# Optimization experiments

Hardware: AMD Instinct MI355X
Metric: run time of the kernel (lower is better)

The kernel has to match this reference:

```python
import jax, jax.numpy as jnp
import numpy as np

HEADS = 8
DIM_HEAD = 64
EPS = 1e-5


def setup_inputs() -> dict:
    key = jax.random.key(0)
    k1, k2, k3, k4 = jax.random.split(key, 4)
    dim, hidden = 256, HEADS * DIM_HEAD
    x = jax.random.normal(k1, (16, dim, 64, 64), dtype=jnp.float32)
    w_qkv = jax.random.normal(k2, (hidden * 3, dim), dtype=jnp.float32) * (dim ** -0.5)
    w_out = jax.random.normal(k3, (dim, hidden), dtype=jnp.float32) * (hidden ** -0.5)
    b_out = jax.random.normal(k4, (dim,), dtype=jnp.float32) * 0.01
    g = jnp.ones((dim,), dtype=jnp.float32)
    return {"x": x, "w_qkv": w_qkv, "w_out": w_out, "b_out": b_out, "g": g}


def reference(x, w_qkv, w_out, b_out, g):
    b, c, H, W = x.shape
    n = H * W
    scale = DIM_HEAD ** -0.5
    xf = x.reshape(b, c, n)
    # 1x1 conv == channel GEMM
    qkv = jnp.einsum('oc,bcn->bon', w_qkv, xf)          # [b, 3*hidden, n]
    q, k, v = jnp.split(qkv, 3, axis=1)
    hd = (b, HEADS, DIM_HEAD, n)
    q = q.reshape(hd)
    k = k.reshape(hd)
    v = v.reshape(hd)
    q = jax.nn.softmax(q, axis=2) * scale               # softmax over head-channel d
    k = jax.nn.softmax(k, axis=3)                       # softmax over tokens n
    v = v / n
    context = jnp.einsum('bhdn,bhen->bhde', k, v)       # [b,h,d,e], d=e=DIM_HEAD
    out = jnp.einsum('bhde,bhdn->bhen', context, q)     # [b,h,e,n]
    out = out.reshape(b, HEADS * DIM_HEAD, n)
    y = jnp.einsum('oc,bcn->bon', w_out, out) + b_out[None, :, None]
    # LayerNorm over channel dim (biased var, eps for fp32)
    mean = jnp.mean(y, axis=1, keepdims=True)
    var = jnp.mean((y - mean) ** 2, axis=1, keepdims=True)
    y = (y - mean) * jax.lax.rsqrt(var + EPS) * g[None, :, None]
    return y.reshape(b, c, H, W)
```

## Files before the change

kernel.cpp:

```cpp
#include <hip/hip_runtime.h>
#include <hip/hip_bf16.h>
#include <cstddef>
#include <cstdint>


typedef __attribute__((ext_vector_type(8))) short s16x8;
typedef __attribute__((ext_vector_type(4))) float f32x4;

#define MFMA(a,b,c) __builtin_amdgcn_mfma_f32_16x16x32_bf16(a,b,c,0,0,0)

#define XT_BSTRIDE 1048576

__device__ __forceinline__ unsigned short f2bf(float f){
    union { float f; unsigned int u; } v; v.f = f;
    unsigned int u = v.u;
    unsigned int r = (u + 0x7FFFu + ((u >> 16) & 1u)) >> 16;
    return (unsigned short)r;
}
__device__ __forceinline__ float bf2f(unsigned short b){
    union { unsigned int u; float f; } v; v.u = ((unsigned int)b) << 16;
    return v.f;
}
__device__ __forceinline__ unsigned int pack2bf(float a, float b){
    __hip_bfloat162 h = __float22bfloat162_rn(make_float2(a, b));
    union { __hip_bfloat162 h; unsigned int u; } v; v.h = h;
    return v.u;
}
__device__ __forceinline__ void gload_lds16(const void* g, void* l){
    __builtin_amdgcn_global_load_lds(
        (const __attribute__((address_space(1))) unsigned int*)g,
        (__attribute__((address_space(3))) unsigned int*)l, 16, 0, 0);
}

__global__ __launch_bounds__(256)
void xprep_kernel(const float* __restrict__ x, unsigned short* __restrict__ XT)
{
    __shared__ float xt[64*68];
    const int tid = threadIdx.x;
    const int n0 = blockIdx.x * 64;
    const int c0 = blockIdx.y * 64;
    const int b  = blockIdx.z;
    {
        const int ci = tid >> 2, ng = tid & 3;
        const float* xs = x + (size_t)b*1048576 + (size_t)(c0+ci)*4096 + n0 + ng*16;
        #pragma unroll
        for (int k=0;k<4;++k){
            float4 v = *(const float4*)(xs + k*4);
            *(float4*)&xt[ci*68 + ng*16 + k*4] = v;
        }
    }
    __syncthreads();
    const int nr = tid >> 2, cg = tid & 3;
    const int n = n0 + nr;
    unsigned short* dstrow = XT + (size_t)b*XT_BSTRIDE + (size_t)n*256;
    #pragma unroll
    for (int t2=0;t2<2;++t2){
        s16x8 pk;
        #pragma unroll
        for (int j=0;j<8;++j){
            int c = cg*16 + t2*8 + j;
            pk[j] = (short)f2bf(xt[c*68 + nr]);
        }
        int blk = (((c0>>3) + cg*2 + t2) ^ (n & 7));
        *(s16x8*)(dstrow + blk*8) = pk;
    }
}

__global__ __launch_bounds__(256)
void wprep_kernel(const float* __restrict__ w, unsigned short* __restrict__ wb)
{
    int i = (blockIdx.x*256 + threadIdx.x) * 8;
    float4 a = *(const float4*)(w + i);
    float4 b = *(const float4*)(w + i + 4);
    s16x8 pk;
    pk[0]=(short)f2bf(a.x); pk[1]=(short)f2bf(a.y); pk[2]=(short)f2bf(a.z); pk[3]=(short)f2bf(a.w);
    pk[4]=(short)f2bf(b.x); pk[5]=(short)f2bf(b.y); pk[6]=(short)f2bf(b.z); pk[7]=(short)f2bf(b.w);
    *(s16x8*)(wb + i) = pk;
}

__global__ __launch_bounds__(256)
void wqprep_kernel(const float* __restrict__ w, unsigned short* __restrict__ wqp)
{
    int t = blockIdx.x*256 + threadIdx.x;
    int row = t >> 5, c8 = t & 31;
    int kc = c8 >> 2, q = c8 & 3;
    const float* src = w + (size_t)row*256 + c8*8;
    float4 a = *(const float4*)(src);
    float4 b = *(const float4*)(src + 4);
    s16x8 pk;
    pk[0]=(short)f2bf(a.x); pk[1]=(short)f2bf(a.y); pk[2]=(short)f2bf(a.z); pk[3]=(short)f2bf(a.w);
    pk[4]=(short)f2bf(b.x); pk[5]=(short)f2bf(b.y); pk[6]=(short)f2bf(b.z); pk[7]=(short)f2bf(b.w);
    *(s16x8*)(wqp + ((size_t)(kc*512 + row)*4 + q)*8) = pk;
}

__global__ __launch_bounds__(256,2)
void kvctx_kernel(const unsigned short* __restrict__ XT, const unsigned short* __restrict__ wb,
                  float* __restrict__ Cp, float* __restrict__ Zp)
{
    extern __shared__ char smraw[];
    unsigned short* xtile = (unsigned short*)smraw;
    unsigned short* kv    = (unsigned short*)(smraw + 32768);

    const int tid = threadIdx.x;
    const int w = tid >> 6, lane = tid & 63;
    const int l15 = lane & 15, q = lane >> 4;
    const int flat = blockIdx.x;
    const int qb  = flat & 63;
    const int h   = flat >> 6;
    const int b   = qb >> 2;
    const int seg = qb & 3;
    const int bh  = b*8 + h;

    s16x8 aW[2][8];
    #pragma unroll
    for (int mf=0;mf<2;++mf){
        int rl = w*16 + l15;
        int grow = (mf==0) ? (512 + h*64 + rl) : (1024 + h*64 + rl);
        const unsigned short* wr = wb + (size_t)grow*256 + q*8;
        #pragma unroll
        for (int kc=0;kc<8;++kc)
            aW[mf][kc] = *(const s16x8*)(wr + kc*32);
    }

    f32x4 ctxacc[4];
    #pragma unroll
    for (int ef=0;ef<4;++ef) ctxacc[ef] = (f32x4){0.f,0.f,0.f,0.f};
    float zacc[4];
    #pragma unroll
    for (int i=0;i<4;++i) zacc[i]=0.f;

    const unsigned short* gsrc0 = XT + (size_t)b*XT_BSTRIDE + (size_t)(seg*1024)*256;

    {
        const unsigned short* gs = gsrc0 + w*4096 + lane*8;
        #pragma unroll
        for (int j=0;j<8;++j)
            gload_lds16(gs + j*512, &xtile[w*4096 + j*512]);
    }
    __syncthreads();

    #pragma unroll 1
    for (int t=0;t<16;++t){
        f32x4 acc[2][4];
        #pragma unroll
        for (int mf=0;mf<2;++mf)
            #pragma unroll
            for (int nf=0;nf<4;++nf) acc[mf][nf]=(f32x4){0.f,0.f,0.f,0.f};
        #pragma unroll
        for (int kc=0;kc<8;++kc){
            s16x8 bf[4];
            #pragma unroll
            for (int nf=0;nf<4;++nf){
                int nl = nf*16 + l15;
                int blk = (kc*4 + q) ^ (nl & 7);
                bf[nf] = *(const s16x8*)&xtile[nl*256 + blk*8];
            }
            #pragma unroll
            for (int mf=0;mf<2;++mf)
                #pragma unroll
                for (int nf=0;nf<4;++nf)
                    acc[mf][nf] = MFMA(aW[mf][kc], bf[nf], acc[mf][nf]);
        }
        #pragma unroll
        for (int mf=0;mf<2;++mf){
            int row = ((mf==0) ? (w*16) : (64 + w*16)) + q*4;
            #pragma unroll
            for (int nf=0;nf<4;++nf){
                int col = nf*16 + l15;
                #pragma unroll
                for (int r=0;r<4;++r){
                    float v = acc[mf][nf][r];
                    unsigned short bv;
                    if (mf == 0){
                        v = __expf(v);
                        bv = f2bf(v);
                        zacc[r] += bf2f(bv);
                    } else {
                        bv = f2bf(v);
                    }
                    kv[(row+r)*72 + col] = bv;
                }
            }
        }
        __syncthreads();
        if (t < 15){
            const unsigned short* gs = gsrc0 + (t+1)*16384 + w*4096 + lane*8;
            #pragma unroll
            for (int j=0;j<8;++j)
                gload_lds16(gs + j*512, &xtile[w*4096 + j*512]);
        }
        #pragma unroll
        for (int kf=0;kf<2;++kf){
            s16x8 aC = *(const s16x8*)&kv[(w*16 + l15)*72 + kf*32 + q*8];
            #pragma unroll
            for (int ef=0;ef<4;++ef){
                s16x8 bC = *(const s16x8*)&kv[(64 + ef*16 + l15)*72 + kf*32 + q*8];
                ctxacc[ef] = MFMA(aC, bC, ctxacc[ef]);
            }
        }
        __syncthreads();
    }

    float* cpb = Cp + (size_t)(bh*4 + seg)*4096;
    #pragma unroll
    for (int ef=0;ef<4;++ef)
        #pragma unroll
        for (int r=0;r<4;++r){
            int d = w*16 + q*4 + r;
            cpb[d*64 + ef*16 + l15] = ctxacc[ef][r];
        }
    #pragma unroll
    for (int i=0;i<4;++i){
        #pragma unroll
        for (int off=1; off<16; off<<=1)
            zacc[i] += __shfl_xor(zacc[i], off, 64);
    }
    if (l15 == 0){
        float* zpb = Zp + (size_t)(bh*4 + seg)*64;
        #pragma unroll
        for (int r=0;r<4;++r)
            zpb[w*16 + q*4 + r] = zacc[r];
    }
}

__global__ __launch_bounds__(512)
void ctxu_kernel(const float* __restrict__ Cp, const float* __restrict__ Zp,
                 const float* __restrict__ wout, unsigned short* __restrict__ U)
{
    extern __shared__ char smraw[];
    float* wl = (float*)smraw;
    float* cl = (float*)(smraw + 69632);
    const int h = blockIdx.x, b = blockIdx.y, tid = threadIdx.x;
    const int bh = b*8 + h;
    {
        const int r = tid >> 1, half = tid & 1;
        const float* wsrc = wout + (size_t)r*512 + h*64 + half*32;
        #pragma unroll
        for (int j=0;j<8;++j){
            float4 v = *(const float4*)(wsrc + j*4);
            *(float4*)&wl[r*68 + half*32 + j*4] = v;
        }
    }
    {
        const int d = tid >> 3, e0 = (tid & 7) * 8;
        float zs = 0.f;
        #pragma unroll
        for (int s=0;s<4;++s) zs += Zp[(bh*4+s)*64 + d];
        float zv = 1.f / (zs * 4096.f);
        const float* cb = Cp + (size_t)(bh*4)*4096 + d*64 + e0;
        float v[8];
        #pragma unroll
        for (int j=0;j<8;++j) v[j]=0.f;
        #pragma unroll
        for (int s=0;s<4;++s){
            float4 t0 = *(const float4*)(cb + (size_t)s*4096);
            float4 t1 = *(const float4*)(cb + (size_t)s*4096 + 4);
            v[0]+=t0.x; v[1]+=t0.y; v[2]+=t0.z; v[3]+=t0.w;
            v[4]+=t1.x; v[5]+=t1.y; v[6]+=t1.z; v[7]+=t1.w;
        }
        #pragma unroll
        for (int j=0;j<8;++j) cl[d*68 + e0 + j] = v[j] * zv;
    }
    __syncthreads();
    const int o = tid & 255, dg = tid >> 8;
    float wlr[64];
    #pragma unroll
    for (int j=0;j<16;++j){
        float4 v = *(const float4*)&wl[o*68 + j*4];
        wlr[j*4+0]=v.x; wlr[j*4+1]=v.y; wlr[j*4+2]=v.z; wlr[j*4+3]=v.w;
    }
    float outv[32];
    #pragma unroll 1
    for (int dd=0;dd<32;++dd){
        const int d = dg*32 + dd;
        float s = 0.f;
        #pragma unroll
        for (int j=0;j<16;++j){
            float4 c4 = *(const float4*)&cl[d*68 + j*4];
            s += wlr[j*4+0]*c4.x + wlr[j*4+1]*c4.y + wlr[j*4+2]*c4.z + wlr[j*4+3]*c4.w;
        }
        outv[dd] = s * 0.125f;
    }
    const int kc = h*2 + dg;
    unsigned short* ub = U + (size_t)b*131072 + (size_t)(kc*256 + o)*32;
    #pragma unroll
    for (int g4=0; g4<4; ++g4){
        uint4 pk;
        pk.x = pack2bf(outv[g4*8+0], outv[g4*8+1]);
        pk.y = pack2bf(outv[g4*8+2], outv[g4*8+3]);
        pk.z = pack2bf(outv[g4*8+4], outv[g4*8+5]);
        pk.w = pack2bf(outv[g4*8+6], outv[g4*8+7]);
        *(uint4*)(ub + g4*8) = pk;
    }
}

__global__ __launch_bounds__(512,4)
void qout_kernel(const unsigned short* __restrict__ XT, const unsigned short* __restrict__ wqp,
                 const unsigned short* __restrict__ U, const float* __restrict__ bout,
                 const float* __restrict__ gg, float* __restrict__ out)
{
    extern __shared__ char smraw[];
    unsigned short* xtile = (unsigned short*)smraw;
    unsigned short* qsm   = (unsigned short*)smraw;
    float* red = (float*)(smraw + 66560);
    float* bl  = (float*)(smraw + 70656);
    float* gl  = (float*)(smraw + 71680);

    const int tid = threadIdx.x;
    const int w = tid >> 6, lane = tid & 63, l15 = lane & 15, q = lane >> 4;
    const int b = blockIdx.y;
    const int n0 = blockIdx.x * 64;

    if (tid < 256){
        bl[tid] = bout[tid];
        gl[tid] = gg[tid];
    }
    {
        const unsigned short* gs = XT + (size_t)b*XT_BSTRIDE + (size_t)n0*256 + w*2048 + lane*8;
        #pragma unroll
        for (int j=0;j<4;++j)
            gload_lds16(gs + j*512, &xtile[w*2048 + j*512]);
    }
    const unsigned short* wqb = wqp + (size_t)q*8 + (size_t)(w*64 + l15)*32;
    s16x8 av0[4];
    #pragma unroll
    for (int mf=0;mf<4;++mf)
        av0[mf] = *(const s16x8*)(wqb + (size_t)mf*16*32);
    __syncthreads();

    f32x4 acc[4][4];
    #pragma unroll
    for (int mf=0;mf<4;++mf)
        #pragma unroll
        for (int nf=0;nf<4;++nf) acc[mf][nf]=(f32x4){0.f,0.f,0.f,0.f};

    #pragma unroll
    for (int kc=0; kc<8; ++kc){
        s16x8 av[4];
        #pragma unroll
        for (int mf=0;mf<4;++mf)
            av[mf] = (kc == 0) ? av0[mf]
                               : *(const s16x8*)(wqb + (size_t)kc*512*32 + (size_t)mf*16*32);
        s16x8 bf[4];
        #pragma unroll
        for (int nf=0;nf<4;++nf){
            int nl = nf*16 + l15;
            int blk = (kc*4 + q) ^ (nl & 7);
            bf[nf] = *(const s16x8*)&xtile[nl*256 + blk*8];
        }
        __builtin_amdgcn_s_setprio(1);
        #pragma unroll
        for (int mf=0;mf<4;++mf)
            #pragma unroll
            for (int nf=0;nf<4;++nf)
                acc[mf][nf] = MFMA(av[mf], bf[nf], acc[mf][nf]);
        __builtin_amdgcn_s_setprio(0);
    }

    #pragma unroll
    for (int nf=0;nf<4;++nf){
        float m = -1e30f;
        #pragma unroll
        for (int mf=0;mf<4;++mf)
            #pragma unroll
            for (int r=0;r<4;++r)
                m = fmaxf(m, acc[mf][nf][r]);
        m = fmaxf(m, __shfl_xor(m, 16, 64));
        m = fmaxf(m, __shfl_xor(m, 32, 64));
        float s = 0.f;
        #pragma unroll
        for (int mf=0;mf<4;++mf)
            #pragma unroll
            for (int r=0;r<4;++r){
                float e = __expf(acc[mf][nf][r] - m);
                acc[mf][nf][r] = e;
                s += e;
            }
        s += __shfl_xor(s, 16, 64);
        s += __shfl_xor(s, 32, 64);
        float rs = 1.f / s;
        #pragma unroll
        for (int mf=0;mf<4;++mf)
            #pragma unroll
            for (int r=0;r<4;++r)
                acc[mf][nf][r] *= rs;
    }
    __syncthreads();

    #pragma unroll
    for (int mf=0;mf<4;++mf){
        int dbase = w*64 + mf*16 + q*4;
        #pragma unroll
        for (int nf=0;nf<4;++nf){
            int n = nf*16 + l15;
            unsigned int lo = pack2bf(acc[mf][nf][0], acc[mf][nf][1]);
            unsigned int hi = pack2bf(acc[mf][nf][2], acc[mf][nf][3]);
            *(uint2*)&qsm[n*520 + dbase] = make_uint2(lo, hi);
        }
    }
    const unsigned short* Ub = U + (size_t)b*131072 + (size_t)q*8 + (size_t)(w*32 + l15)*32;
    s16x8 uvP[4];
    #pragma unroll
    for (int i=0;i<4;++i)
        uvP[i] = *(const s16x8*)(Ub + (size_t)(i>>1)*256*32 + (size_t)(i&1)*16*32);
    __syncthreads();

    f32x4 yacc[2][4];
    #pragma unroll
    for (int mf=0;mf<2;++mf)
        #pragma unroll
        for (int nf=0;nf<4;++nf) yacc[mf][nf]=(f32x4){0.f,0.f,0.f,0.f};

    #pragma unroll
    for (int kc=0; kc<16; ++kc){
        s16x8 uv[2];
        #pragma unroll
        for (int mf=0;mf<2;++mf)
            uv[mf] = (kc < 2) ? uvP[(kc<<1)|mf]
                              : *(const s16x8*)(Ub + (size_t)kc*256*32 + (size_t)mf*16*32);
        s16x8 bf[4];
        #pragma unroll
        for (int nf=0;nf<4;++nf){
            int n = nf*16 + l15;
            bf[nf] = *(const s16x8*)&qsm[n*520 + kc*32 + q*8];
        }
        __builtin_amdgcn_s_setprio(1);
        #pragma unroll
        for (int mf=0;mf<2;++mf)
            #pragma unroll
            for (int nf=0;nf<4;++nf)
                yacc[mf][nf] = MFMA(uv[mf], bf[nf], yacc[mf][nf]);
        __builtin_amdgcn_s_setprio(0);
    }

    #pragma unroll
    for (int mf=0;mf<2;++mf){
        int ob = w*32 + mf*16 + q*4;
        #pragma unroll
        for (int r=0;r<4;++r){
            float bo = bl[ob + r];
            #pragma unroll
            for (int nf=0;nf<4;++nf) yacc[mf][nf][r] += bo;
        }
    }
    float s1[4], s2[4];
    #pragma unroll
    for (int nf=0;nf<4;++nf){ s1[nf]=0.f; s2[nf]=0.f; }
    #pragma unroll
    for (int mf=0;mf<2;++mf)
        #pragma unroll
        for (int nf=0;nf<4;++nf)
            #pragma unroll
            for (int r=0;r<4;++r){
                float v = yacc[mf][nf][r];
                s1[nf] += v; s2[nf] += v*v;
            }
    #pragma unroll
    for (int nf=0;nf<4;++nf){
        s1[nf] += __shfl_xor(s1[nf], 16, 64);
        s1[nf] += __shfl_xor(s1[nf], 32, 64);
        s2[nf] += __shfl_xor(s2[nf], 16, 64);
        s2[nf] += __shfl_xor(s2[nf], 32, 64);
    }
    if (q == 0){
        #pragma unroll
        for (int nf=0;nf<4;++nf){
            int col = nf*16 + l15;
            red[(w*64 + col)*2 + 0] = s1[nf];
            red[(w*64 + col)*2 + 1] = s2[nf];
        }
    }
    __syncthreads();
    float mean_[4], inv_[4];
    #pragma unroll
    for (int nf=0;nf<4;++nf){
        int col = nf*16 + l15;
        float S1 = 0.f, S2 = 0.f;
        #pragma unroll
        for (int w2=0; w2<8; ++w2){
            S1 += red[(w2*64 + col)*2 + 0];
            S2 += red[(w2*64 + col)*2 + 1];
        }
        float mn = S1 * (1.f/256.f);
        float vr = S2 * (1.f/256.f) - mn*mn;
        mean_[nf] = mn;
        inv_[nf] = rsqrtf(vr + 1e-5f);
    }
    float* ob = out + (size_t)b*1048576 + n0;
    #pragma unroll
    for (int mf=0;mf<2;++mf){
        #pragma unroll
        for (int r=0;r<4;++r){
            int o = w*32 + mf*16 + q*4 + r;
            float gv = gl[o];
            #pragma unroll
            for (int nf=0;nf<4;++nf){
                float val = (yacc[mf][nf][r] - mean_[nf]) * inv_[nf] * gv;
                ob[(size_t)o*4096 + nf*16 + l15] = val;
            }
        }
    }
}

extern "C" void kernel_launch(void* const* d_in, const int* in_sizes, int n_in,
                              void* d_out, int out_size, void* d_ws, size_t ws_size,
                              hipStream_t stream)
{
    const float* x    = (const float*)d_in[0];
    const float* wqkv = (const float*)d_in[1];
    const float* wout = (const float*)d_in[2];
    const float* bout = (const float*)d_in[3];
    const float* g    = (const float*)d_in[4];
    float* out = (float*)d_out;

    char* wsb = (char*)d_ws;
    unsigned short* XTs = (unsigned short*)wsb;
    unsigned short* wbf = (unsigned short*)(wsb + 33554432);
    unsigned short* Upk = (unsigned short*)(wsb + 34340864);
    float* Cp  = (float*)(wsb + 38535168);
    float* Zp  = (float*)(wsb + 46923776);
    unsigned short* wqp = (unsigned short*)(wsb + 47054848);

    hipLaunchKernelGGL(xprep_kernel,  dim3(64, 4, 16), dim3(256), 0,     stream, x, XTs);
    hipLaunchKernelGGL(wprep_kernel,  dim3(192),       dim3(256), 0,     stream, wqkv, wbf);
    hipLaunchKernelGGL(wqprep_kernel, dim3(64),        dim3(256), 0,     stream, wqkv, wqp);
    hipLaunchKernelGGL(kvctx_kernel,  dim3(512),       dim3(256), 51200, stream, XTs, wbf, Cp, Zp);
    hipLaunchKernelGGL(ctxu_kernel,   dim3(8, 16),     dim3(512), 87040, stream, Cp, Zp, wout, Upk);
    hipLaunchKernelGGL(qout_kernel,   dim3(64, 16),    dim3(512), 72704, stream, XTs, wqp, Upk, bout, g, out);
}
```

Measured before the change: 138.0 us.

## Split kvctx work across 8 waves: separate K and V projection waves

The kvctx kernel moves from 256 to 512 threads per block. Waves 0-3 compute the K projection (exp and row-sum) and waves 4-7 compute the V projection, where before each wave did both. The context MFMA is split by output column halves across the two wave groups. This halves per-wave register use and MFMA work, adding latency hiding and parallelism within each block, at the cost of more waves contending for LDS and the same barrier count.

After: 146.4 us. 1.06x slower.

```diff
diff --git a/kernel.cpp b/kernel.cpp
--- a/kernel.cpp
+++ b/kernel.cpp
@@ -93,7 +93,7 @@
     *(s16x8*)(wqp + ((size_t)(kc*512 + row)*4 + q)*8) = pk;
 }
 
-__global__ __launch_bounds__(256,2)
+__global__ __launch_bounds__(512,4)
 void kvctx_kernel(const unsigned short* __restrict__ XT, const unsigned short* __restrict__ wb,
                   float* __restrict__ Cp, float* __restrict__ Zp)
 {
@@ -104,6 +104,8 @@
     const int tid = threadIdx.x;
     const int w = tid >> 6, lane = tid & 63;
     const int l15 = lane & 15, q = lane >> 4;
+    const int isK = (w < 4);
+    const int wf  = w & 3;
     const int flat = blockIdx.x;
     const int qb  = flat & 63;
     const int h   = flat >> 6;
@@ -111,20 +113,19 @@
     const int seg = qb & 3;
     const int bh  = b*8 + h;
 
-    s16x8 aW[2][8];
-    #pragma unroll
-    for (int mf=0;mf<2;++mf){
-        int rl = w*16 + l15;
-        int grow = (mf==0) ? (512 + h*64 + rl) : (1024 + h*64 + rl);
+    s16x8 aW[8];
+    {
+        int rl = wf*16 + l15;
+        int grow = isK ? (512 + h*64 + rl) : (1024 + h*64 + rl);
         const unsigned short* wr = wb + (size_t)grow*256 + q*8;
         #pragma unroll
         for (int kc=0;kc<8;++kc)
-            aW[mf][kc] = *(const s16x8*)(wr + kc*32);
-    }
-
-    f32x4 ctxacc[4];
-    #pragma unroll
-    for (int ef=0;ef<4;++ef) ctxacc[ef] = (f32x4){0.f,0.f,0.f,0.f};
+            aW[kc] = *(const s16x8*)(wr + kc*32);
+    }
+
+    f32x4 ctxacc[2];
+    ctxacc[0]=(f32x4){0.f,0.f,0.f,0.f};
+    ctxacc[1]=(f32x4){0.f,0.f,0.f,0.f};
     float zacc[4];
     #pragma unroll
     for (int i=0;i<4;++i) zacc[i]=0.f;
@@ -132,20 +133,18 @@
     const unsigned short* gsrc0 = XT + (size_t)b*XT_BSTRIDE + (size_t)(seg*1024)*256;
 
     {
-        const unsigned short* gs = gsrc0 + w*4096 + lane*8;
-        #pragma unroll
-        for (int j=0;j<8;++j)
-            gload_lds16(gs + j*512, &xtile[w*4096 + j*512]);
+        const unsigned short* gs = gsrc0 + w*2048 + lane*8;
+        #pragma unroll
+        for (int j=0;j<4;++j)
+            gload_lds16(gs + j*512, &xtile[w*2048 + j*512]);
     }
     __syncthreads();
 
     #pragma unroll 1
     for (int t=0;t<16;++t){
-        f32x4 acc[2][4];
-        #pragma unroll
-        for (int mf=0;mf<2;++mf)
-            #pragma unroll
-            for (int nf=0;nf<4;++nf) acc[mf][nf]=(f32x4){0.f,0.f,0.f,0.f};
+        f32x4 acc[4];
+        #pragma unroll
+        for (int nf=0;nf<4;++nf) acc[nf]=(f32x4){0.f,0.f,0.f,0.f};
         #pragma unroll
         for (int kc=0;kc<8;++kc){
             s16x8 bf[4];
@@ -156,22 +155,19 @@
                 bf[nf] = *(const s16x8*)&xtile[nl*256 + blk*8];
             }
             #pragma unroll
-            for (int mf=0;mf<2;++mf)
-                #pragma unroll
-                for (int nf=0;nf<4;++nf)
-                    acc[mf][nf] = MFMA(aW[mf][kc], bf[nf], acc[mf][nf]);
-        }
-        #pragma unroll
-        for (int mf=0;mf<2;++mf){
-            int row = ((mf==0) ? (w*16) : (64 + w*16)) + q*4;
+            for (int nf=0;nf<4;++nf)
+                acc[nf] = MFMA(aW[kc], bf[nf], acc[nf]);
+        }
+        {
+            int row = (isK ? (wf*16) : (64 + wf*16)) + q*4;
             #pragma unroll
             for (int nf=0;nf<4;++nf){
                 int col = nf*16 + l15;
                 #pragma unroll
                 for (int r=0;r<4;++r){
-                    float v = acc[mf][nf][r];
+                    float v = acc[nf][r];
                     unsigned short bv;
-                    if (mf == 0){
+                    if (isK){
                         v = __expf(v);
                         bv = f2bf(v);
                         zacc[r] += bf2f(bv);
@@ -184,17 +180,18 @@
         }
         __syncthreads();
         if (t < 15){
-            const unsigned short* gs = gsrc0 + (t+1)*16384 + w*4096 + lane*8;
-            #pragma unroll
-            for (int j=0;j<8;++j)
-                gload_lds16(gs + j*512, &xtile[w*4096 + j*512]);
+            const unsigned short* gs = gsrc0 + (t+1)*16384 + w*2048 + lane*8;
+            #pragma unroll
+            for (int j=0;j<4;++j)
+                gload_lds16(gs + j*512, &xtile[w*2048 + j*512]);
         }
         #pragma unroll
         for (int kf=0;kf<2;++kf){
-            s16x8 aC = *(const s16x8*)&kv[(w*16 + l15)*72 + kf*32 + q*8];
-            #pragma unroll
-            for (int ef=0;ef<4;++ef){
-                s16x8 bC = *(const s16x8*)&kv[(64 + ef*16 + l15)*72 + kf*32 + q*8];
+            s16x8 aC = *(const s16x8*)&kv[(wf*16 + l15)*72 + kf*32 + q*8];
+            #pragma unroll
+            for (int ef=0;ef<2;++ef){
+                int e = (w>>2)*32 + ef*16 + l15;
+                s16x8 bC = *(const s16x8*)&kv[(64 + e)*72 + kf*32 + q*8];
                 ctxacc[ef] = MFMA(aC, bC, ctxacc[ef]);
             }
         }
@@ -203,23 +200,26 @@
 
     float* cpb = Cp + (size_t)(bh*4 + seg)*4096;
     #pragma unroll
-    for (int ef=0;ef<4;++ef)
+    for (int ef=0;ef<2;++ef)
         #pragma unroll
         for (int r=0;r<4;++r){
-            int d = w*16 + q*4 + r;
-            cpb[d*64 + ef*16 + l15] = ctxacc[ef][r];
-        }
-    #pragma unroll
-    for (int i=0;i<4;++i){
-        #pragma unroll
-        for (int off=1; off<16; off<<=1)
-            zacc[i] += __shfl_xor(zacc[i], off, 64);
-    }
-    if (l15 == 0){
-        float* zpb = Zp + (size_t)(bh*4 + seg)*64;
-        #pragma unroll
-        for (int r=0;r<4;++r)
-            zpb[w*16 + q*4 + r] = zacc[r];
+            int d = wf*16 + q*4 + r;
+            int e = (w>>2)*32 + ef*16 + l15;
+            cpb[d*64 + e] = ctxacc[ef][r];
+        }
+    if (isK){
+        #pragma unroll
+        for (int i=0;i<4;++i){
+            #pragma unroll
+            for (int off=1; off<16; off<<=1)
+                zacc[i] += __shfl_xor(zacc[i], off, 64);
+        }
+        if (l15 == 0){
+            float* zpb = Zp + (size_t)(bh*4 + seg)*64;
+            #pragma unroll
+            for (int r=0;r<4;++r)
+                zpb[wf*16 + q*4 + r] = zacc[r];
+        }
     }
 }
 
@@ -524,7 +524,7 @@
     hipLaunchKernelGGL(xprep_kernel,  dim3(64, 4, 16), dim3(256), 0,     stream, x, XTs);
     hipLaunchKernelGGL(wprep_kernel,  dim3(192),       dim3(256), 0,     stream, wqkv, wbf);
     hipLaunchKernelGGL(wqprep_kernel, dim3(64),        dim3(256), 0,     stream, wqkv, wqp);
-    hipLaunchKernelGGL(kvctx_kernel,  dim3(512),       dim3(256), 51200, stream, XTs, wbf, Cp, Zp);
+    hipLaunchKernelGGL(kvctx_kernel,  dim3(512),       dim3(512), 51200, stream, XTs, wbf, Cp, Zp);
     hipLaunchKernelGGL(ctxu_kernel,   dim3(8, 16),     dim3(512), 87040, stream, Cp, Zp, wout, Upk);
     hipLaunchKernelGGL(qout_kernel,   dim3(64, 16),    dim3(512), 72704, stream, XTs, wqp, Upk, bout, g, out);
 }
```
